# Kernel optimization log

Hardware: AMD Instinct MI355X
Metric: run time of the kernel (lower is better)

Reference implementation:

```python
import math
import jax, jax.numpy as jnp
import numpy as np

N_HEAD = 16
N_EMBD = 1024
HEAD_DIM = N_EMBD // N_HEAD  # 64
SHARED = 16
PRIV = HEAD_DIM - SHARED     # 48
B, T = 4, 2048
STD = 0.02


def setup_inputs() -> dict:
    key = jax.random.key(0)
    ks = jax.random.split(key, 6)
    x = jax.random.normal(ks[0], (B, T, N_EMBD), dtype=jnp.float32)
    # Linear params stored as (in, out); bias zeros per _reset_parameters
    W_share = jax.random.normal(ks[1], (N_EMBD, SHARED), dtype=jnp.float32) * STD
    Wq = jax.random.normal(ks[2], (N_EMBD, N_HEAD * PRIV), dtype=jnp.float32) * STD
    Wk = jax.random.normal(ks[3], (N_EMBD, N_HEAD * PRIV), dtype=jnp.float32) * STD
    Wv = jax.random.normal(ks[4], (N_EMBD, N_EMBD), dtype=jnp.float32) * STD
    Wo = jax.random.normal(ks[5], (N_EMBD, N_EMBD), dtype=jnp.float32) * STD
    return {
        'hidden_states': x,
        'W_share': W_share, 'b_share': jnp.zeros((SHARED,), jnp.float32),
        'Wq': Wq, 'bq': jnp.zeros((N_HEAD * PRIV,), jnp.float32),
        'Wk': Wk, 'bk': jnp.zeros((N_HEAD * PRIV,), jnp.float32),
        'Wv': Wv, 'bv': jnp.zeros((N_EMBD,), jnp.float32),
        'Wo': Wo, 'bo': jnp.zeros((N_EMBD,), jnp.float32),
    }


def reference(hidden_states, W_share, b_share, Wq, bq, Wk, bk, Wv, bv, Wo, bo):
    x = hidden_states
    Bt, Tt, C = x.shape
    # shared projection, broadcast across heads: (B,T,s) -> (B,H,T,s)
    share = x @ W_share + b_share
    share_h = jnp.broadcast_to(share[:, None, :, :], (Bt, N_HEAD, Tt, SHARED))
    # private q/k: (B,T,H*p) -> (B,H,T,p)
    q_priv = (x @ Wq + bq).reshape(Bt, Tt, N_HEAD, PRIV).transpose(0, 2, 1, 3)
    k_priv = (x @ Wk + bk).reshape(Bt, Tt, N_HEAD, PRIV).transpose(0, 2, 1, 3)
    q = jnp.concatenate([share_h, q_priv], axis=-1)  # (B,H,T,head_dim)
    k = jnp.concatenate([share_h, k_priv], axis=-1)
    v = (x @ Wv + bv).reshape(Bt, Tt, N_HEAD, HEAD_DIM).transpose(0, 2, 1, 3)
    scale = 1.0 / math.sqrt(HEAD_DIM)
    att = jnp.einsum('bhqd,bhkd->bhqk', q, k) * scale
    causal = jnp.tril(jnp.ones((Tt, Tt), dtype=bool))
    att = jnp.where(causal[None, None, :, :], att, -jnp.inf)
    att = jax.nn.softmax(att, axis=-1)
    y = jnp.einsum('bhqk,bhkd->bhqd', att, v)
    y = y.transpose(0, 2, 1, 3).reshape(Bt, Tt, C)
    y = y @ Wo + bo
    return y
```

## Files before the change

kernel.cpp:

```cpp
#include <hip/hip_runtime.h>
#include <hip/hip_bf16.h>

typedef unsigned short u16;
typedef short short8 __attribute__((ext_vector_type(8)));
typedef float f32x4 __attribute__((ext_vector_type(4)));

#define N_EMBD   1024
#define N_HEADS  16
#define HEAD_DIM 64
#define PRIV     48
#define SEQ_T    2048
#define BATCH    4
#define M_ROWS   (BATCH*SEQ_T)
#define PNS      2688
#define NTILES   (SEQ_T/64)

#if __has_builtin(__builtin_amdgcn_exp2f)
#define EXP2(x) __builtin_amdgcn_exp2f(x)
#else
#define EXP2(x) exp2f(x)
#endif

#if __has_builtin(__builtin_amdgcn_global_load_lds)
#define HAVE_GLL 1
#else
#define HAVE_GLL 0
#endif

__device__ __forceinline__ u16 f2bf(float f) {
  __hip_bfloat16 h = __float2bfloat16(f);
  return *reinterpret_cast<u16*>(&h);
}
__device__ __forceinline__ float bf2f(u16 s) {
  __hip_bfloat16 h;
  *reinterpret_cast<u16*>(&h) = s;
  return __bfloat162float(h);
}
__device__ __forceinline__ float loadv(const void* p, size_t i, int isf32) {
  return isf32 ? ((const float*)p)[i] : bf2f(((const u16*)p)[i]);
}
__device__ __forceinline__ u16 truncbf(float f) {
  unsigned u = __builtin_bit_cast(unsigned, f);
  return (u16)(u >> 16);
}
#if HAVE_GLL
__device__ __forceinline__ void gload_lds16(const u16* g, u16* l) {
  __builtin_amdgcn_global_load_lds(
      (const __attribute__((address_space(1))) void*)g,
      (__attribute__((address_space(3))) void*)l, 16, 0, 0);
}
#endif

__global__ __launch_bounds__(256) void detect_kernel(const u16* __restrict__ x,
                                                     int* __restrict__ flag) {
  __shared__ int cnt;
  if (threadIdx.x == 0) cnt = 0;
  __syncthreads();
  u16 v = x[2 * threadIdx.x];
  int e = (v >> 7) & 0xFF;
  int junk = (e >= 0xC0 || (e != 0 && e <= 0x30)) ? 1 : 0;
  if (junk) atomicAdd(&cnt, 1);
  __syncthreads();
  if (threadIdx.x == 0) *flag = (cnt > 16) ? 1 : 0;
}

__global__ __launch_bounds__(256) void pack_t_kernel(
    const void* __restrict__ Wsh, const void* __restrict__ Wq,
    const void* __restrict__ Wk,  const void* __restrict__ Wv,
    const void* __restrict__ Wo,
    const void* __restrict__ bsh, const void* __restrict__ bq,
    const void* __restrict__ bk,  const void* __restrict__ bv,
    const void* __restrict__ bo,
    u16* __restrict__ Wcat, u16* __restrict__ Woc,
    u16* __restrict__ bcat, u16* __restrict__ boc,
    const int* __restrict__ flagp)
{
  const int f = *flagp;
  if (blockIdx.z == 5) {
    const int flat = blockIdx.y * 16 + blockIdx.x;
    const int padN = (PNS - 2576) * 1024;
    for (int i = flat * 256 + threadIdx.x; i < padN; i += 256 * 256)
      Wcat[(size_t)2576 * 1024 + i] = 0;
    if (flat == 0) {
      for (int c = threadIdx.x; c < PNS; c += 256) {
        float v = 0.f;
        if (c < 16)        v = loadv(bsh, c, f);
        else if (c < 784)  v = loadv(bq, c - 16, f);
        else if (c < 1552) v = loadv(bk, c - 784, f);
        else if (c < 2576) v = loadv(bv, c - 1552, f);
        bcat[c] = f2bf(v);
      }
    } else if (flat == 1) {
      for (int c = threadIdx.x; c < N_EMBD; c += 256)
        boc[c] = f2bf(loadv(bo, c, f));
    }
    return;
  }
  const void* src; u16* dst; int N, rowOff;
  switch (blockIdx.z) {
    case 0: src = Wsh; dst = Wcat; N = 16;   rowOff = 0;    break;
    case 1: src = Wq;  dst = Wcat; N = 768;  rowOff = 16;   break;
    case 2: src = Wk;  dst = Wcat; N = 768;  rowOff = 784;  break;
    case 3: src = Wv;  dst = Wcat; N = 1024; rowOff = 1552; break;
    default:src = Wo;  dst = Woc;  N = 1024; rowOff = 0;    break;
  }
  const int n0 = blockIdx.x * 64;
  if (n0 >= N) return;
  const int k0 = blockIdx.y * 64;
  __shared__ u16 t[64][65];
  const int tx = threadIdx.x & 63, ty = threadIdx.x >> 6;
#pragma unroll
  for (int rr = 0; rr < 16; rr++) {
    int k = k0 + ty * 16 + rr;
    int n = n0 + tx;
    float v = (n < N) ? loadv(src, (size_t)k * N + n, f) : 0.f;
    t[ty * 16 + rr][tx] = f2bf(v);
  }
  __syncthreads();
#pragma unroll
  for (int rr = 0; rr < 16; rr++) {
    int n = ty * 16 + rr;
    if (n0 + n < N)
      dst[(size_t)(rowOff + n0 + n) * 1024 + k0 + tx] = t[tx][n];
  }
}

__global__ __launch_bounds__(256) void vt_kernel(const u16* __restrict__ P,
                                                 u16* __restrict__ Vt)
{
  const int tt = blockIdx.x * 64;
  const int bh = blockIdx.y;
  const int b = bh >> 4, h = bh & 15;
  const int vcol = 1552 + h * HEAD_DIM;
  __shared__ u16 t[64][65];
  const int tx = threadIdx.x & 63, ty = threadIdx.x >> 6;
#pragma unroll
  for (int rr = 0; rr < 16; rr++) {
    int r = ty * 16 + rr;
    t[r][tx] = P[((size_t)b * SEQ_T + tt + r) * PNS + vcol + tx];
  }
  __syncthreads();
#pragma unroll
  for (int rr = 0; rr < 16; rr++) {
    int d = ty * 16 + rr;
    Vt[((size_t)bh * 64 + d) * SEQ_T + tt + tx] = t[tx][d];
  }
}

template <bool AF32>
__global__ __launch_bounds__(256, 3) void gemm_bias_kernel(
    const void* __restrict__ A, int lda,
    const u16* __restrict__ Bt,
    const u16* __restrict__ bias,
    void* __restrict__ C, int ldc, int K,
    const int* __restrict__ flagp, int a_dyn, int c_dyn)
{
  const int isf = *flagp;
  if (AF32 != (a_dyn != 0 && isf != 0)) return;
  const bool cf32 = (c_dyn != 0) && (isf != 0);

  __shared__ __align__(16) u16 As[2][128 * 32];
  __shared__ __align__(16) u16 Bs[2][128 * 32];
  const int tid  = threadIdx.x;
  const int lane = tid & 63;
  const int w    = tid >> 6;
  const int quad = lane >> 4;
  const int l16  = lane & 15;

  const int bid = blockIdx.x;
  const int xcd = bid & 7;
  const int s   = bid >> 3;
  const int mb  = xcd * 8 + (s & 7);
  const int nb  = s >> 3;
  const int m0  = mb * 128;
  const int n0  = nb * 128;
  const int wm  = (w >> 1) * 64;
  const int wn  = (w & 1) * 64;

  int mS[2], lgS[2];
#pragma unroll
  for (int i = 0; i < 2; i++) {
    int c  = tid + i * 256;
    int m  = c >> 2;
    int pc = c & 3;
    mS[i]  = m;
    lgS[i] = (pc ^ (m & 3) ^ ((m >> 2) & 3)) * 8;
  }

  const u16* A16  = (const u16*)A;
  const float* A32 = (const float*)A;

#define STAGE(k0, bb)                                                          \
  {                                                                            \
    _Pragma("unroll") for (int i = 0; i < 2; i++) {                            \
      int c = tid + i * 256;                                                   \
      if (AF32) {                                                              \
        const float* srcp = A32 + (size_t)(m0 + mS[i]) * lda + (k0) + lgS[i];  \
        float4 v0 = *(const float4*)srcp;                                      \
        float4 v1 = *(const float4*)(srcp + 4);                                \
        u16 tb[8];                                                             \
        tb[0] = f2bf(v0.x); tb[1] = f2bf(v0.y); tb[2] = f2bf(v0.z);            \
        tb[3] = f2bf(v0.w); tb[4] = f2bf(v1.x); tb[5] = f2bf(v1.y);            \
        tb[6] = f2bf(v1.z); tb[7] = f2bf(v1.w);                                \
        *(uint4*)&As[bb][c * 8] = *(const uint4*)tb;                           \
        *(uint4*)&Bs[bb][c * 8] =                                              \
            *(const uint4*)(Bt + (size_t)(n0 + mS[i]) * K + (k0) + lgS[i]);    \
      } else {                                                                 \
        GLOAD(A16 + (size_t)(m0 + mS[i]) * lda + (k0) + lgS[i], &As[bb][c*8]); \
        GLOAD(Bt + (size_t)(n0 + mS[i]) * K + (k0) + lgS[i], &Bs[bb][c*8]);    \
      }                                                                        \
    }                                                                          \
  }
#if HAVE_GLL
#define GLOAD(g, l) gload_lds16((g), (l))
#else
#define GLOAD(g, l) (*(uint4*)(l) = *(const uint4*)(g))
#endif

  f32x4 acc[4][4];
#pragma unroll
  for (int i = 0; i < 4; i++)
#pragma unroll
    for (int j = 0; j < 4; j++) acc[i][j] = (f32x4){0.f, 0.f, 0.f, 0.f};

  const int swr = (quad ^ (l16 & 3) ^ ((l16 >> 2) & 3)) * 8;

  STAGE(0, 0);
  __syncthreads();

  const int NIT = K / 32;
  for (int kt = 0; kt < NIT; kt++) {
    const int cur = kt & 1;
    if (kt + 1 < NIT) STAGE((kt + 1) * 32, 1 - cur);

    short8 af[4], bfr[4];
#pragma unroll
    for (int mt = 0; mt < 4; mt++)
      af[mt] = *(const short8*)&As[cur][(wm + mt * 16 + l16) * 32 + swr];
#pragma unroll
    for (int nt = 0; nt < 4; nt++)
      bfr[nt] = *(const short8*)&Bs[cur][(wn + nt * 16 + l16) * 32 + swr];
#pragma unroll
    for (int mt = 0; mt < 4; mt++)
#pragma unroll
      for (int nt = 0; nt < 4; nt++)
        acc[mt][nt] = __builtin_amdgcn_mfma_f32_16x16x32_bf16(af[mt], bfr[nt], acc[mt][nt], 0, 0, 0);

    if (kt + 1 < NIT) __syncthreads();
  }
#undef STAGE
#undef GLOAD

#pragma unroll
  for (int nt = 0; nt < 4; nt++) {
    int col  = n0 + wn + nt * 16 + l16;
    float bv = bf2f(bias[col]);
#pragma unroll
    for (int mt = 0; mt < 4; mt++) {
#pragma unroll
      for (int r = 0; r < 4; r++) {
        int row   = m0 + wm + mt * 16 + quad * 4 + r;
        float val = acc[mt][nt][r] + bv;
        if (cf32) ((float*)C)[(size_t)row * ldc + col] = val;
        else      ((u16*)C)[(size_t)row * ldc + col]   = f2bf(val);
      }
    }
  }
}

__global__ __launch_bounds__(256, 3) void attn_kernel(
    const u16* __restrict__ P, const u16* __restrict__ Vt,
    u16* __restrict__ Y)
{
  const int bh  = blockIdx.x;
  const int b   = bh >> 4, h = bh & 15;
  const int p   = blockIdx.y;
  const int qtA = p, qtB = NTILES - 1 - p;
  const int tid = threadIdx.x;
  const int w   = tid >> 6;
  const int lane = tid & 63;
  const int quad = lane >> 4, l16 = lane & 15;
  const size_t rowb = (size_t)b * SEQ_T;
  const int qcol = 16 + h * PRIV;
  const int kcol = 784 + h * PRIV;

  __shared__ __align__(16) u16 Ks[2][64 * 64];
  __shared__ __align__(16) u16 Vs[2][64 * 64];
  __shared__ __align__(16) u16 Ps[4][2][16 * 68];

  const float csc = 0.18033688011112042f;
  const int d0  = quad * 8;
  const int cq0 = (d0 < 16) ? d0 : (qcol + d0 - 16);
  const int iA = qtA * 64 + w * 16, iB = qtB * 64 + w * 16;
  const u16* qrowA = P + (rowb + iA + l16) * PNS;
  const u16* qrowB = P + (rowb + iB + l16) * PNS;
  short8 qaA0 = *(const short8*)&qrowA[cq0];
  short8 qaA1 = *(const short8*)&qrowA[qcol + 16 + d0];
  short8 qaB0 = *(const short8*)&qrowB[cq0];
  short8 qaB1 = *(const short8*)&qrowB[qcol + 16 + d0];
#pragma unroll
  for (int e = 0; e < 8; e++) {
    qaA0[e] = (short)f2bf(bf2f((u16)qaA0[e]) * csc);
    qaA1[e] = (short)f2bf(bf2f((u16)qaA1[e]) * csc);
    qaB0[e] = (short)f2bf(bf2f((u16)qaB0[e]) * csc);
    qaB1[e] = (short)f2bf(bf2f((u16)qaB1[e]) * csc);
  }
  short8 ones;
#pragma unroll
  for (int e = 0; e < 8; e++) ones[e] = (short)0x3F80;

#if HAVE_GLL
#define GLOADA(g, l) gload_lds16((g), (l))
#else
#define GLOADA(g, l) (*(uint4*)(l) = *(const uint4*)(g))
#endif
#define STAGE_KV(k0, bb)                                                       \
  {                                                                            \
    _Pragma("unroll") for (int i2 = 0; i2 < 2; i2++) {                         \
      int c   = tid + i2 * 256;                                                \
      int row = c >> 3;                                                        \
      int dg  = ((c & 7) ^ (row & 7)) * 8;                                     \
      int col = (dg < 16) ? dg : (kcol + dg - 16);                             \
      GLOADA(&P[(rowb + (k0) + row) * PNS + col], &Ks[bb][c * 8]);             \
      GLOADA(&Vt[((size_t)bh * 64 + row) * SEQ_T + (k0) + dg], &Vs[bb][c * 8]);\
    }                                                                          \
  }

  f32x4 accyA[4], accyB[4], acclA, acclB;
#pragma unroll
  for (int g = 0; g < 4; g++) {
    accyA[g] = (f32x4){0.f, 0.f, 0.f, 0.f};
    accyB[g] = (f32x4){0.f, 0.f, 0.f, 0.f};
  }
  acclA = (f32x4){0.f, 0.f, 0.f, 0.f};
  acclB = (f32x4){0.f, 0.f, 0.f, 0.f};

  const int nkt = qtB + 1;
  STAGE_KV(0, 0);
  __syncthreads();

  for (int kt = 0; kt < nkt; kt++) {
    const int cur = kt & 1;
    const int k0  = kt * 64;
    if (kt + 1 < nkt) STAGE_KV((kt + 1) * 64, 1 - cur);

    const bool doA = (kt <= qtA);

    float svA[4][4], svB[4][4];
#pragma unroll
    for (int g = 0; g < 4; g++) {
      int j = g * 16 + l16;
      short8 kb0 = *(const short8*)&Ks[cur][j * 64 + ((quad    ) ^ (j & 7)) * 8];
      short8 kb1 = *(const short8*)&Ks[cur][j * 64 + ((quad + 4) ^ (j & 7)) * 8];
      f32x4 sB = (f32x4){0.f, 0.f, 0.f, 0.f};
      sB = __builtin_amdgcn_mfma_f32_16x16x32_bf16(qaB0, kb0, sB, 0, 0, 0);
      sB = __builtin_amdgcn_mfma_f32_16x16x32_bf16(qaB1, kb1, sB, 0, 0, 0);
#pragma unroll
      for (int r = 0; r < 4; r++) svB[g][r] = sB[r];
      if (doA) {
        f32x4 sA = (f32x4){0.f, 0.f, 0.f, 0.f};
        sA = __builtin_amdgcn_mfma_f32_16x16x32_bf16(qaA0, kb0, sA, 0, 0, 0);
        sA = __builtin_amdgcn_mfma_f32_16x16x32_bf16(qaA1, kb1, sA, 0, 0, 0);
#pragma unroll
        for (int r = 0; r < 4; r++) svA[g][r] = sA[r];
      }
    }
    if (kt == qtA && doA) {
#pragma unroll
      for (int g = 0; g < 4; g++)
#pragma unroll
        for (int r = 0; r < 4; r++) {
          int gi = iA + quad * 4 + r;
          int gj = k0 + g * 16 + l16;
          if (gj > gi) svA[g][r] = -__builtin_inff();
        }
    }
    if (kt == qtB) {
#pragma unroll
      for (int g = 0; g < 4; g++)
#pragma unroll
        for (int r = 0; r < 4; r++) {
          int gi = iB + quad * 4 + r;
          int gj = k0 + g * 16 + l16;
          if (gj > gi) svB[g][r] = -__builtin_inff();
        }
    }

    if (doA) {
#pragma unroll
      for (int g = 0; g < 4; g++)
#pragma unroll
        for (int r = 0; r < 4; r++)
          Ps[w][0][(quad * 4 + r) * 68 + g * 16 + l16] = truncbf(EXP2(svA[g][r]));
    }
#pragma unroll
    for (int g = 0; g < 4; g++)
#pragma unroll
      for (int r = 0; r < 4; r++)
        Ps[w][1][(quad * 4 + r) * 68 + g * 16 + l16] = truncbf(EXP2(svB[g][r]));

#pragma unroll
    for (int kf = 0; kf < 2; kf++) {
      short8 vb[4];
#pragma unroll
      for (int g2 = 0; g2 < 4; g2++) {
        int row = g2 * 16 + l16;
        vb[g2] = *(const short8*)&Vs[cur][row * 64 + (((kf * 4 + quad) ^ (row & 7)) * 8)];
      }
      short8 paB = *(const short8*)&Ps[w][1][l16 * 68 + kf * 32 + quad * 8];
      acclB = __builtin_amdgcn_mfma_f32_16x16x32_bf16(paB, ones, acclB, 0, 0, 0);
#pragma unroll
      for (int g2 = 0; g2 < 4; g2++)
        accyB[g2] = __builtin_amdgcn_mfma_f32_16x16x32_bf16(paB, vb[g2], accyB[g2], 0, 0, 0);
      if (doA) {
        short8 paA = *(const short8*)&Ps[w][0][l16 * 68 + kf * 32 + quad * 8];
        acclA = __builtin_amdgcn_mfma_f32_16x16x32_bf16(paA, ones, acclA, 0, 0, 0);
#pragma unroll
        for (int g2 = 0; g2 < 4; g2++)
          accyA[g2] = __builtin_amdgcn_mfma_f32_16x16x32_bf16(paA, vb[g2], accyA[g2], 0, 0, 0);
      }
    }

    if (kt + 1 < nkt) __syncthreads();
  }
#undef STAGE_KV
#undef GLOADA

  float invA[4], invB[4];
#pragma unroll
  for (int r = 0; r < 4; r++) {
    invA[r] = 1.0f / acclA[r];
    invB[r] = 1.0f / acclB[r];
  }
#pragma unroll
  for (int g2 = 0; g2 < 4; g2++) {
    int col = h * HEAD_DIM + g2 * 16 + l16;
#pragma unroll
    for (int r = 0; r < 4; r++) {
      int giA = iA + quad * 4 + r;
      int giB = iB + quad * 4 + r;
      Y[(rowb + giA) * N_EMBD + col] = f2bf(accyA[g2][r] * invA[r]);
      Y[(rowb + giB) * N_EMBD + col] = f2bf(accyB[g2][r] * invB[r]);
    }
  }
}

extern "C" void kernel_launch(void* const* d_in, const int* in_sizes, int n_in,
                              void* d_out, int out_size, void* d_ws, size_t ws_size,
                              hipStream_t stream) {
  (void)in_sizes; (void)n_in; (void)out_size; (void)ws_size;
  const void* x   = d_in[0];
  const void* Wsh = d_in[1];
  const void* bsh = d_in[2];
  const void* Wq  = d_in[3];
  const void* bq  = d_in[4];
  const void* Wk  = d_in[5];
  const void* bk  = d_in[6];
  const void* Wv  = d_in[7];
  const void* bv  = d_in[8];
  const void* Wo  = d_in[9];
  const void* bo  = d_in[10];

  char* wsb = (char*)d_ws;
  int* flag = (int*)wsb;
  u16* ws16 = (u16*)(wsb + 64);
  u16* Wcat = ws16;
  u16* bcat = Wcat + (size_t)PNS * N_EMBD;
  u16* Woc  = bcat + PNS;
  u16* boc  = Woc + (size_t)N_EMBD * N_EMBD;
  u16* Pb   = boc + N_EMBD;
  u16* Yb   = Pb + (size_t)M_ROWS * PNS;
  u16* Vtb  = Yb + (size_t)M_ROWS * N_EMBD;

  detect_kernel<<<dim3(1), dim3(256), 0, stream>>>((const u16*)x, flag);
  pack_t_kernel<<<dim3(16, 16, 6), dim3(256), 0, stream>>>(
      Wsh, Wq, Wk, Wv, Wo, bsh, bq, bk, bv, bo, Wcat, Woc, bcat, boc, flag);
  gemm_bias_kernel<false><<<dim3(64 * (PNS / 128)), dim3(256), 0, stream>>>(
      x, N_EMBD, Wcat, bcat, Pb, PNS, N_EMBD, flag, 1, 0);
  gemm_bias_kernel<true><<<dim3(64 * (PNS / 128)), dim3(256), 0, stream>>>(
      x, N_EMBD, Wcat, bcat, Pb, PNS, N_EMBD, flag, 1, 0);
  vt_kernel<<<dim3(SEQ_T / 64, BATCH * N_HEADS), dim3(256), 0, stream>>>(
      Pb, Vtb);
  attn_kernel<<<dim3(BATCH * N_HEADS, NTILES / 2), dim3(256), 0, stream>>>(
      Pb, Vtb, Yb);
  gemm_bias_kernel<false><<<dim3(64 * (N_EMBD / 128)), dim3(256), 0, stream>>>(
      Yb, N_EMBD, Woc, boc, d_out, N_EMBD, N_EMBD, flag, 0, 1);
}
```

Measured before the change: 306.1 us.

## Replace GEMMs with 8-wave 128x256 triple-buffered kernel and pre-convert input to bf16

Both projection GEMMs move from a 256-thread, 128x128, double-buffered K=32 kernel to a 512-thread, 128x256-tile kernel. The new kernel uses K=64 steps, triple-buffered global-to-LDS loads, explicit waitcnt and barrier scheduling, MFMA priority hints, and an LDS-staged vectorized epilogue. The fp32 input is converted to bf16 once in a separate pass into the Y buffer, so the GEMM no longer needs an fp32-A path. PNS is padded to 2816 so it divides evenly by 256, which adds some wasted columns and an extra conversion pass in exchange for larger tiles and better latency hiding.

```diff
diff --git a/kernel.cpp b/kernel.cpp
--- a/kernel.cpp
+++ b/kernel.cpp
@@ -12,8 +12,9 @@
 #define SEQ_T    2048
 #define BATCH    4
 #define M_ROWS   (BATCH*SEQ_T)
-#define PNS      2688
+#define PNS      2816
 #define NTILES   (SEQ_T/64)
+#define NT_K     16
 
 #if __has_builtin(__builtin_amdgcn_exp2f)
 #define EXP2(x) __builtin_amdgcn_exp2f(x)
@@ -125,6 +126,194 @@
   }
 }
 
+__global__ __launch_bounds__(256) void xbf_kernel(const void* __restrict__ x,
+                                                  u16* __restrict__ Xb,
+                                                  const int* __restrict__ flagp) {
+  const int f = *flagp;
+  const size_t i = (size_t)blockIdx.x * 256 + threadIdx.x;
+  if (f) {
+    const float4* p = (const float4*)x;
+    float4 a = p[i * 2], b = p[i * 2 + 1];
+    u16 t[8] = {f2bf(a.x), f2bf(a.y), f2bf(a.z), f2bf(a.w),
+                f2bf(b.x), f2bf(b.y), f2bf(b.z), f2bf(b.w)};
+    *(uint4*)&Xb[i * 8] = *(const uint4*)t;
+  } else {
+    *(uint4*)&Xb[i * 8] = ((const uint4*)x)[i];
+  }
+}
+
+__global__ __launch_bounds__(512, 2) void gemm8p_kernel(
+    const u16* __restrict__ A,
+    const u16* __restrict__ Bt,
+    const u16* __restrict__ bias,
+    void* __restrict__ C, int ldc, int Mtiles,
+    const int* __restrict__ flagp, int c_dyn)
+{
+  __shared__ __align__(16) u16 smem[73728];
+  u16* const As = smem;
+  u16* const Bs = smem + 3 * 8192;
+
+  const bool cf32 = (c_dyn != 0) && (*flagp != 0);
+
+  const int tid  = threadIdx.x;
+  const int lane = tid & 63;
+  const int w    = tid >> 6;
+  const int quad = lane >> 4, l16 = lane & 15;
+  const int wm   = w >> 2, wn = w & 3;
+
+  const int nwg = gridDim.x;
+  const int wg  = (blockIdx.x & 7) * (nwg >> 3) + (blockIdx.x >> 3);
+  const int mb  = wg % Mtiles, nb = wg / Mtiles;
+  const int m0  = mb * 128, n0 = nb * 256;
+
+  int ldsA[2]; size_t glA[2];
+  int ldsB[2][2]; size_t glB[2][2];
+#pragma unroll
+  for (int rd = 0; rd < 2; rd++) {
+    int j = tid + rd * 512, rp = j >> 3, s = j & 7;
+    int cl = (s ^ (rp & 7)) * 8;
+    ldsA[rd] = rp * 64 + s * 8;
+    glA[rd]  = (size_t)(m0 + rp) * 1024 + cl;
+#pragma unroll
+    for (int nh = 0; nh < 2; nh++) {
+      int cc = (rp & 31) + nh * 32 + (rp >> 5) * 64;
+      ldsB[nh][rd] = cc * 64 + s * 8;
+      glB[nh][rd]  = (size_t)(n0 + cc) * 1024 + cl;
+    }
+  }
+
+#if HAVE_GLL
+#define G8(g, l) gload_lds16((g), (l))
+#else
+#define G8(g, l) (*(uint4*)(l) = *(const uint4*)(g))
+#endif
+#define STG_A(t, bf)                                                       \
+  if ((t) < NT_K) {                                                        \
+    _Pragma("unroll") for (int rd = 0; rd < 2; rd++)                       \
+      G8(A + glA[rd] + (t) * 64, As + (bf) * 8192 + ldsA[rd]);             \
+  }
+#define STG_B(nh, t, bf)                                                   \
+  if ((t) < NT_K) {                                                        \
+    _Pragma("unroll") for (int rd = 0; rd < 2; rd++)                       \
+      G8(Bt + glB[nh][rd] + (t) * 64, Bs + (bf) * 16384 + ldsB[nh][rd]);   \
+  }
+
+  const int ck0  = ((quad)     ^ (l16 & 7)) * 8;
+  const int ck1  = ((4 + quad) ^ (l16 & 7)) * 8;
+  const int arow = (wm * 64 + l16) * 64;
+  const int brow = (wn * 64 + l16) * 64;
+
+  f32x4 acc[4][4];
+#pragma unroll
+  for (int i = 0; i < 4; i++)
+#pragma unroll
+    for (int j = 0; j < 4; j++) acc[i][j] = (f32x4){0.f, 0.f, 0.f, 0.f};
+
+  short8 af[4][2], bA[2][2], bB[2][2];
+
+#define READ_A(cur)                                                        \
+  { const u16* pa = As + (cur) * 8192 + arow;                              \
+    _Pragma("unroll") for (int m = 0; m < 4; m++) {                        \
+      af[m][0] = *(const short8*)(pa + m * 1024 + ck0);                    \
+      af[m][1] = *(const short8*)(pa + m * 1024 + ck1); } }
+#define READ_B(dst, nh, cur)                                               \
+  { const u16* pb = Bs + (cur) * 16384 + brow + (nh) * 2048;               \
+    _Pragma("unroll") for (int n = 0; n < 2; n++) {                        \
+      dst[n][0] = *(const short8*)(pb + n * 1024 + ck0);                   \
+      dst[n][1] = *(const short8*)(pb + n * 1024 + ck1); } }
+#define MM16(bfr, nh)                                                      \
+  __builtin_amdgcn_s_setprio(1);                                           \
+  _Pragma("unroll") for (int m = 0; m < 4; m++)                            \
+    _Pragma("unroll") for (int n = 0; n < 2; n++) {                        \
+      acc[m][(nh)*2+n] = __builtin_amdgcn_mfma_f32_16x16x32_bf16(          \
+          af[m][0], bfr[n][0], acc[m][(nh)*2+n], 0, 0, 0);                 \
+      acc[m][(nh)*2+n] = __builtin_amdgcn_mfma_f32_16x16x32_bf16(          \
+          af[m][1], bfr[n][1], acc[m][(nh)*2+n], 0, 0, 0); }               \
+  __builtin_amdgcn_s_setprio(0);
+#define BARR { __builtin_amdgcn_s_barrier(); __builtin_amdgcn_sched_barrier(0); }
+
+  STG_A(0, 0); STG_B(1, 0, 0); STG_B(0, 0, 0);
+  STG_A(1, 1); STG_B(1, 1, 1); STG_B(0, 1, 1);
+  asm volatile("s_waitcnt vmcnt(6)");
+  BARR;
+
+#pragma unroll
+  for (int kt = 0; kt < NT_K; kt++) {
+    const int cur = kt % 3;
+    const int stb = (kt + 2) % 3;
+    READ_A(cur); READ_B(bA, 0, cur);
+    STG_A(kt + 2, stb); STG_B(1, kt + 2, stb);
+    BARR;
+    MM16(bA, 0);
+    BARR;
+    READ_B(bB, 1, cur);
+    STG_B(0, kt + 2, stb);
+    BARR;
+    MM16(bB, 1);
+    if (kt < NT_K - 2)       { asm volatile("s_waitcnt vmcnt(6)"); }
+    else if (kt == NT_K - 2) { asm volatile("s_waitcnt vmcnt(0)"); }
+    BARR;
+  }
+#undef STG_A
+#undef STG_B
+#undef READ_A
+#undef READ_B
+#undef MM16
+#undef BARR
+#undef G8
+
+  float bvv[4];
+#pragma unroll
+  for (int ni = 0; ni < 4; ni++)
+    bvv[ni] = bf2f(bias[n0 + wn * 64 + ni * 16 + l16]);
+
+  if (!cf32) {
+    u16* cs = smem + w * 4096;
+#pragma unroll
+    for (int m = 0; m < 4; m++)
+#pragma unroll
+      for (int ni = 0; ni < 4; ni++)
+#pragma unroll
+        for (int r = 0; r < 4; r++) {
+          int row = m * 16 + quad * 4 + r;
+          int ch  = ((ni * 2 + (l16 >> 3)) ^ (row & 7)) * 8 + (l16 & 7);
+          cs[row * 64 + ch] = f2bf(acc[m][ni][r] + bvv[ni]);
+        }
+    u16* Cb = (u16*)C;
+#pragma unroll
+    for (int i = 0; i < 8; i++) {
+      int ch = lane + i * 64;
+      int rr = ch >> 3, cc = ch & 7;
+      short8 v = *(const short8*)(cs + rr * 64 + ((cc ^ (rr & 7)) * 8));
+      *(short8*)&Cb[(size_t)(m0 + wm * 64 + rr) * ldc + n0 + wn * 64 + cc * 8] = v;
+    }
+  } else {
+    float* cf = (float*)(void*)smem + w * 2048;
+#pragma unroll
+    for (int pass = 0; pass < 2; pass++) {
+#pragma unroll
+      for (int m2 = 0; m2 < 2; m2++)
+#pragma unroll
+        for (int ni = 0; ni < 4; ni++)
+#pragma unroll
+          for (int r = 0; r < 4; r++) {
+            int row = m2 * 16 + quad * 4 + r;
+            int ch  = ((ni * 4 + (l16 >> 2)) ^ (row & 15)) * 4 + (l16 & 3);
+            cf[row * 64 + ch] = acc[pass * 2 + m2][ni][r] + bvv[ni];
+          }
+      float* Cf = (float*)C;
+#pragma unroll
+      for (int i = 0; i < 8; i++) {
+        int ch = lane + i * 64;
+        int rr = ch >> 4, cc = ch & 15;
+        f32x4 v = *(const f32x4*)(cf + rr * 64 + ((cc ^ (rr & 15)) * 4));
+        *(f32x4*)&Cf[(size_t)(m0 + wm * 64 + pass * 32 + rr) * ldc +
+                     n0 + wn * 64 + cc * 4] = v;
+      }
+    }
+  }
+}
+
 __global__ __launch_bounds__(256) void vt_kernel(const u16* __restrict__ P,
                                                  u16* __restrict__ Vt)
 {
@@ -144,127 +333,6 @@
   for (int rr = 0; rr < 16; rr++) {
     int d = ty * 16 + rr;
     Vt[((size_t)bh * 64 + d) * SEQ_T + tt + tx] = t[tx][d];
-  }
-}
-
-template <bool AF32>
-__global__ __launch_bounds__(256, 3) void gemm_bias_kernel(
-    const void* __restrict__ A, int lda,
-    const u16* __restrict__ Bt,
-    const u16* __restrict__ bias,
-    void* __restrict__ C, int ldc, int K,
-    const int* __restrict__ flagp, int a_dyn, int c_dyn)
-{
-  const int isf = *flagp;
-  if (AF32 != (a_dyn != 0 && isf != 0)) return;
-  const bool cf32 = (c_dyn != 0) && (isf != 0);
-
-  __shared__ __align__(16) u16 As[2][128 * 32];
-  __shared__ __align__(16) u16 Bs[2][128 * 32];
-  const int tid  = threadIdx.x;
-  const int lane = tid & 63;
-  const int w    = tid >> 6;
-  const int quad = lane >> 4;
-  const int l16  = lane & 15;
-
-  const int bid = blockIdx.x;
-  const int xcd = bid & 7;
-  const int s   = bid >> 3;
-  const int mb  = xcd * 8 + (s & 7);
-  const int nb  = s >> 3;
-  const int m0  = mb * 128;
-  const int n0  = nb * 128;
-  const int wm  = (w >> 1) * 64;
-  const int wn  = (w & 1) * 64;
-
-  int mS[2], lgS[2];
-#pragma unroll
-  for (int i = 0; i < 2; i++) {
-    int c  = tid + i * 256;
-    int m  = c >> 2;
-    int pc = c & 3;
-    mS[i]  = m;
-    lgS[i] = (pc ^ (m & 3) ^ ((m >> 2) & 3)) * 8;
-  }
-
-  const u16* A16  = (const u16*)A;
-  const float* A32 = (const float*)A;
-
-#define STAGE(k0, bb)                                                          \
-  {                                                                            \
-    _Pragma("unroll") for (int i = 0; i < 2; i++) {                            \
-      int c = tid + i * 256;                                                   \
-      if (AF32) {                                                              \
-        const float* srcp = A32 + (size_t)(m0 + mS[i]) * lda + (k0) + lgS[i];  \
-        float4 v0 = *(const float4*)srcp;                                      \
-        float4 v1 = *(const float4*)(srcp + 4);                                \
-        u16 tb[8];                                                             \
-        tb[0] = f2bf(v0.x); tb[1] = f2bf(v0.y); tb[2] = f2bf(v0.z);            \
-        tb[3] = f2bf(v0.w); tb[4] = f2bf(v1.x); tb[5] = f2bf(v1.y);            \
-        tb[6] = f2bf(v1.z); tb[7] = f2bf(v1.w);                                \
-        *(uint4*)&As[bb][c * 8] = *(const uint4*)tb;                           \
-        *(uint4*)&Bs[bb][c * 8] =                                              \
-            *(const uint4*)(Bt + (size_t)(n0 + mS[i]) * K + (k0) + lgS[i]);    \
-      } else {                                                                 \
-        GLOAD(A16 + (size_t)(m0 + mS[i]) * lda + (k0) + lgS[i], &As[bb][c*8]); \
-        GLOAD(Bt + (size_t)(n0 + mS[i]) * K + (k0) + lgS[i], &Bs[bb][c*8]);    \
-      }                                                                        \
-    }                                                                          \
-  }
-#if HAVE_GLL
-#define GLOAD(g, l) gload_lds16((g), (l))
-#else
-#define GLOAD(g, l) (*(uint4*)(l) = *(const uint4*)(g))
-#endif
-
-  f32x4 acc[4][4];
-#pragma unroll
-  for (int i = 0; i < 4; i++)
-#pragma unroll
-    for (int j = 0; j < 4; j++) acc[i][j] = (f32x4){0.f, 0.f, 0.f, 0.f};
-
-  const int swr = (quad ^ (l16 & 3) ^ ((l16 >> 2) & 3)) * 8;
-
-  STAGE(0, 0);
-  __syncthreads();
-
-  const int NIT = K / 32;
-  for (int kt = 0; kt < NIT; kt++) {
-    const int cur = kt & 1;
-    if (kt + 1 < NIT) STAGE((kt + 1) * 32, 1 - cur);
-
-    short8 af[4], bfr[4];
-#pragma unroll
-    for (int mt = 0; mt < 4; mt++)
-      af[mt] = *(const short8*)&As[cur][(wm + mt * 16 + l16) * 32 + swr];
-#pragma unroll
-    for (int nt = 0; nt < 4; nt++)
-      bfr[nt] = *(const short8*)&Bs[cur][(wn + nt * 16 + l16) * 32 + swr];
-#pragma unroll
-    for (int mt = 0; mt < 4; mt++)
-#pragma unroll
-      for (int nt = 0; nt < 4; nt++)
-        acc[mt][nt] = __builtin_amdgcn_mfma_f32_16x16x32_bf16(af[mt], bfr[nt], acc[mt][nt], 0, 0, 0);
-
-    if (kt + 1 < NIT) __syncthreads();
-  }
-#undef STAGE
-#undef GLOAD
-
-#pragma unroll
-  for (int nt = 0; nt < 4; nt++) {
-    int col  = n0 + wn + nt * 16 + l16;
-    float bv = bf2f(bias[col]);
-#pragma unroll
-    for (int mt = 0; mt < 4; mt++) {
-#pragma unroll
-      for (int r = 0; r < 4; r++) {
-        int row   = m0 + wm + mt * 16 + quad * 4 + r;
-        float val = acc[mt][nt][r] + bv;
-        if (cf32) ((float*)C)[(size_t)row * ldc + col] = val;
-        else      ((u16*)C)[(size_t)row * ldc + col]   = f2bf(val);
-      }
-    }
   }
 }
 
@@ -471,18 +539,19 @@
   u16* Pb   = boc + N_EMBD;
   u16* Yb   = Pb + (size_t)M_ROWS * PNS;
   u16* Vtb  = Yb + (size_t)M_ROWS * N_EMBD;
+  u16* Xb   = Yb;
 
   detect_kernel<<<dim3(1), dim3(256), 0, stream>>>((const u16*)x, flag);
   pack_t_kernel<<<dim3(16, 16, 6), dim3(256), 0, stream>>>(
       Wsh, Wq, Wk, Wv, Wo, bsh, bq, bk, bv, bo, Wcat, Woc, bcat, boc, flag);
-  gemm_bias_kernel<false><<<dim3(64 * (PNS / 128)), dim3(256), 0, stream>>>(
-      x, N_EMBD, Wcat, bcat, Pb, PNS, N_EMBD, flag, 1, 0);
-  gemm_bias_kernel<true><<<dim3(64 * (PNS / 128)), dim3(256), 0, stream>>>(
-      x, N_EMBD, Wcat, bcat, Pb, PNS, N_EMBD, flag, 1, 0);
+  xbf_kernel<<<dim3(M_ROWS * N_EMBD / (256 * 8)), dim3(256), 0, stream>>>(
+      x, Xb, flag);
+  gemm8p_kernel<<<dim3(64 * (PNS / 256)), dim3(512), 0, stream>>>(
+      Xb, Wcat, bcat, Pb, PNS, 64, flag, 0);
   vt_kernel<<<dim3(SEQ_T / 64, BATCH * N_HEADS), dim3(256), 0, stream>>>(
       Pb, Vtb);
   attn_kernel<<<dim3(BATCH * N_HEADS, NTILES / 2), dim3(256), 0, stream>>>(
       Pb, Vtb, Yb);
-  gemm_bias_kernel<false><<<dim3(64 * (N_EMBD / 128)), dim3(256), 0, stream>>>(
-      Yb, N_EMBD, Woc, boc, d_out, N_EMBD, N_EMBD, flag, 0, 1);
-}
+  gemm8p_kernel<<<dim3(64 * (N_EMBD / 256)), dim3(512), 0, stream>>>(
+      Yb, Woc, boc, d_out, N_EMBD, 64, flag, 1);
+}
```

Result: faster. 291.5 us (-4.8%).
